# Kernel optimization log

Measured on AMD Instinct MI355X. Metric: run time of the kernel, lower is better.

Reference implementation:

```python
import jax, jax.numpy as jnp
import numpy as np

RES = 64
C_DIM = 64
N_BLOCKS = 4
EPS = 1e-12


def conv2d(x, w, b, pad):
    out = jax.lax.conv_general_dilated(
        x, w, window_strides=(1, 1), padding=[(pad, pad), (pad, pad)],
        dimension_numbers=('NCHW', 'OIHW', 'NCHW'))
    return out + b[None, :, None, None]


def unfold3(x):
    # F.unfold(kernel=3, padding=1): [B,C,H,W] -> [B, C*9, H*W], torch ordering (c, ki, kj)
    B, C, H, W = x.shape
    xp = jnp.pad(x, ((0, 0), (0, 0), (1, 1), (1, 1)))
    patches = jnp.stack([xp[:, :, ki:ki + H, kj:kj + W]
                         for ki in range(3) for kj in range(3)], axis=2)  # [B,C,9,H,W]
    return patches.reshape(B, C * 9, H * W)


def fold3(t, H, W):
    # F.fold(kernel=3, padding=1): sum overlapping patches back to [B,C,H,W]
    B, C9, L = t.shape
    C = C9 // 9
    t = t.reshape(B, C, 3, 3, H, W)
    out = jnp.zeros((B, C, H + 2, W + 2), t.dtype)
    for ki in range(3):
        for kj in range(3):
            out = out.at[:, :, ki:ki + H, kj:kj + W].add(t[:, :, ki, kj])
    return out[:, :, 1:H + 1, 1:W + 1]


def setup_inputs() -> dict:
    key = jax.random.key(0)
    ks = jax.random.split(key, 16)
    B, L, C = 4, RES * RES, C_DIM
    s = 0.05
    inp = {
        'c0': jax.random.normal(ks[0], (B, L, C), jnp.float32),
        'f0': jax.random.normal(ks[1], (B, L, C), jnp.float32),
        'c1': jax.random.normal(ks[2], (B, L, C), jnp.float32),
        'head_w': jax.random.normal(ks[3], (C, C, 5, 5), jnp.float32) * s,
        'head_b': jax.random.normal(ks[4], (C,), jnp.float32) * s,
        'rb_w1': jax.random.normal(ks[5], (N_BLOCKS, C, C, 3, 3), jnp.float32) * s,
        'rb_b1': jax.random.normal(ks[6], (N_BLOCKS, C), jnp.float32) * s,
        'rb_w2': jax.random.normal(ks[7], (N_BLOCKS, C, C, 3, 3), jnp.float32) * s,
        'rb_b2': jax.random.normal(ks[8], (N_BLOCKS, C), jnp.float32) * s,
        'tail_w': jax.random.normal(ks[9], (C, C, 5, 5), jnp.float32) * s,
        'tail_b': jax.random.normal(ks[10], (C,), jnp.float32) * s,
        'sq_w': jax.random.normal(ks[11], (C, 2 * C, 5, 5), jnp.float32) * s,
        'sq_b': jax.random.normal(ks[12], (C,), jnp.float32) * s,
    }
    return inp


def reference(c0, f0, c1, head_w, head_b, rb_w1, rb_b1, rb_w2, rb_b2,
              tail_w, tail_b, sq_w, sq_b):
    B, L, C = c1.shape
    H = W = RES
    c1 = c1.swapaxes(1, 2).reshape(B, C, H, W)
    c0 = c0.swapaxes(1, 2).reshape(B, C, H, W)
    f0 = f0.swapaxes(1, 2).reshape(B, C, H, W)
    Delta_c = c1 - c0

    # --- search_Trans: patch correlation + best-match texture transfer ---
    c1u = unfold3(c1)                       # [B, C9, L]
    c0u = unfold3(c0).swapaxes(1, 2)        # [B, L, C9]
    c0n = c0u / jnp.maximum(jnp.linalg.norm(c0u, axis=2, keepdims=True), EPS)
    c1n = c1u / jnp.maximum(jnp.linalg.norm(c1u, axis=1, keepdims=True), EPS)
    R = jnp.einsum('blk,bkm->blm', c0n, c1n)  # [B, L, L]
    R_star = jnp.max(R, axis=1)               # [B, L]
    R_arg = jnp.argmax(R, axis=1)              # [B, L]
    f0u = unfold3(f0)                          # [B, C9, L]
    Tu = jnp.take_along_axis(f0u, R_arg[:, None, :], axis=2)
    T = fold3(Tu, H, W) / 9.0                  # [B, C, H, W]
    S = R_star.reshape(B, 1, H, W)

    # --- residual conv stack on Delta_c ---
    x1 = conv2d(Delta_c, head_w, head_b, 2)
    x = x1
    for i in range(rb_w1.shape[0]):  # NOTE: original feeds x1 into every block
        h = jax.nn.relu(conv2d(x1, rb_w1[i], rb_b1[i], 1))
        x = conv2d(h, rb_w2[i], rb_b2[i], 1) + x1
    x = conv2d(x, tail_w, tail_b, 2)
    Delta_c_fea = x + x1

    x = conv2d(jnp.concatenate([Delta_c_fea, T], axis=1), sq_w, sq_b, 2)
    out = Delta_c_fea + x * S
    return out.reshape(B, C, L).swapaxes(1, 2)
```

## Files before the change

### kernel.cpp

```cpp
#include <hip/hip_runtime.h>
#include <hip/hip_bf16.h>


#define BATCH 4

typedef unsigned short u16;
typedef unsigned int   u32;
typedef __attribute__((ext_vector_type(8))) short short8;
typedef __attribute__((ext_vector_type(4))) float f32x4;

__device__ __forceinline__ void bsplit2(float a, float b, u32& ho, u32& lo) {
  __hip_bfloat16 ha = __float2bfloat16(a), hb = __float2bfloat16(b);
  float ra = a - __bfloat162float(ha), rb = b - __bfloat162float(hb);
  __hip_bfloat16 la = __float2bfloat16(ra), lb = __float2bfloat16(rb);
  ho = (u32)*(u16*)&ha | ((u32)*(u16*)&hb << 16);
  lo = (u32)*(u16*)&la | ((u32)*(u16*)&lb << 16);
}

__device__ __forceinline__ void gload_lds16(const void* g, void* l) {
  __builtin_amdgcn_global_load_lds((const __attribute__((address_space(1))) void*)g,
                                   (__attribute__((address_space(3))) void*)l, 16, 0, 0);
}

__global__ __launch_bounds__(256) void prep_ss(const float* __restrict__ c0,
    const float* __restrict__ c1, float* __restrict__ ss0, float* __restrict__ ss1)
{
  int tid = blockIdx.x * 256 + threadIdx.x;
  const float* p0 = c0 + (size_t)tid * 64;
  const float* p1 = c1 + (size_t)tid * 64;
  float s0 = 0.f, s1 = 0.f;
  for (int c = 0; c < 64; ++c) {
    float a = p0[c]; s0 += a * a;
    float b = p1[c]; s1 += b * b;
  }
  ss0[tid] = s0;
  ss1[tid] = s1;
}

__global__ __launch_bounds__(256) void norm_kernel(const float* __restrict__ ss0,
    const float* __restrict__ ss1, float* __restrict__ inv0, float* __restrict__ inv1)
{
  int tid = blockIdx.x * 256 + threadIdx.x;
  int b = tid >> 12, l = tid & 4095;
  int y = l >> 6, x = l & 63;
  int base = b << 12;
  float s0 = 0.f, s1 = 0.f;
  for (int dy = -1; dy <= 1; ++dy) {
    int yy = y + dy; if (yy < 0 || yy >= 64) continue;
    for (int dx = -1; dx <= 1; ++dx) {
      int xx = x + dx; if (xx < 0 || xx >= 64) continue;
      int ii = base + (yy << 6) + xx;
      s0 += ss0[ii]; s1 += ss1[ii];
    }
  }
  inv0[tid] = 1.f / fmaxf(sqrtf(s0), 1e-12f);
  inv1[tid] = 1.f / fmaxf(sqrtf(s1), 1e-12f);
}

__global__ __launch_bounds__(256) void split_pad_kernel(const float* __restrict__ c0,
    const float* __restrict__ c1, u16* __restrict__ p0h, u16* __restrict__ p0l,
    u16* __restrict__ p1h, u16* __restrict__ p1l)
{
  int b = blockIdx.y, t = threadIdx.x;
  int pix = blockIdx.x * 4 + (t >> 6);
  int c = t & 63;
  int py = pix / 66, px = pix - py * 66;
  size_t d = ((size_t)b * 4356 + pix) * 64 + c;
  float v0 = 0.f, v1 = 0.f;
  if (py >= 1 && py <= 64 && px >= 1 && px <= 64) {
    size_t s = (((size_t)b << 12) + ((py - 1) << 6) + (px - 1)) * 64 + c;
    v0 = c0[s]; v1 = c1[s];
  }
  __hip_bfloat16 h = __float2bfloat16(v0);
  float r = v0 - __bfloat162float(h);
  __hip_bfloat16 lo = __float2bfloat16(r);
  p0h[d] = *(u16*)&h; p0l[d] = *(u16*)&lo;
  h = __float2bfloat16(v1);
  r = v1 - __bfloat162float(h);
  lo = __float2bfloat16(r);
  p1h[d] = *(u16*)&h; p1l[d] = *(u16*)&lo;
}

__global__ __launch_bounds__(256) void wprep(const float* __restrict__ src,
    u16* __restrict__ wh, u16* __restrict__ wl, int Cin, int KK, int n)
{
  int i = blockIdx.x * 256 + threadIdx.x;
  if (i >= n) return;
  int per = Cin * KK;
  int cout = i / per;
  int rem = i - cout * per;
  int cin = rem / KK;
  int tap = rem - cin * KK;
  float x = src[i];
  __hip_bfloat16 h = __float2bfloat16(x);
  float r = x - __bfloat162float(h);
  __hip_bfloat16 lo = __float2bfloat16(r);
  int d = (tap * 64 + cout) * Cin + cin;
  wh[d] = *(u16*)&h;
  wl[d] = *(u16*)&lo;
}

__global__ __launch_bounds__(256) void corr_mfma(const u16* __restrict__ p0h,
    const u16* __restrict__ p0l, const u16* __restrict__ p1h, const u16* __restrict__ p1l,
    const float* __restrict__ inv0, float* __restrict__ pval, int* __restrict__ pidx)
{
  __shared__ __align__(16) u16 smem[16384];
  int mt = blockIdx.x, lt = blockIdx.y, b = blockIdx.z;
  int t = threadIdx.x;
  int lane = t & 63, w = t >> 6;
  int wl = w >> 1, wm = w & 1;
  int cc = lane & 15, q = lane >> 4;
  const size_t boff = (size_t)b * 278784;
  const u16* msrc = (w == 0) ? p0h : (w == 1) ? p0l : (w == 2) ? p1h : p1l;
  msrc += boff;
  const float* inv0b = inv0 + (b << 12);
  u16* ldsm = smem + (w << 12);
  int isB = w >> 1;

  int srow0 = lane >> 2;
  int cs_g  = (lane & 3) ^ ((lane >> 3) & 3);
  int sw    = (cc >> 1) & 3;

  float bval[4] = {-1e30f, -1e30f, -1e30f, -1e30f};
  int   bidx[4] = {0, 0, 0, 0};

  for (int sub = 0; sub < 4; ++sub) {
    int row0 = (lt << 9) + (sub << 7);
    int pb = isB ? (mt << 7) : row0;
    f32x4 acc[4][4];
#pragma unroll
    for (int i = 0; i < 4; ++i)
#pragma unroll
      for (int j = 0; j < 4; ++j) acc[i][j] = (f32x4){0.f, 0.f, 0.f, 0.f};

    for (int ph = 0; ph < 18; ++ph) {
      int r = ph >> 1, hh = ph & 1;
      int ki = r / 3, kj = r - ki * 3;
      __syncthreads();
#pragma unroll
      for (int it = 0; it < 8; ++it) {
        int row = (it << 4) + srow0;
        int p = pb + row;
        int ypad = (p >> 6) + ki, xpad = (p & 63) + kj;
        const u16* g = msrc + (((size_t)(ypad * 66 + xpad)) << 6) + (hh << 5) + (cs_g << 3);
        gload_lds16(g, ldsm + (it << 9));
      }
      __syncthreads();
      short8 afh[4], afl[4], bfh[4], bfl[4];
#pragma unroll
      for (int i = 0; i < 4; ++i) {
        int ra = (((wl << 6) + (i << 4) + cc) << 5) + ((q ^ sw) << 3);
        afh[i] = *(const short8*)(&smem[ra]);
        afl[i] = *(const short8*)(&smem[4096 + ra]);
      }
#pragma unroll
      for (int j = 0; j < 4; ++j) {
        int rb = (((wm << 6) + (j << 4) + cc) << 5) + ((q ^ sw) << 3);
        bfh[j] = *(const short8*)(&smem[8192 + rb]);
        bfl[j] = *(const short8*)(&smem[12288 + rb]);
      }
#pragma unroll
      for (int i = 0; i < 4; ++i)
#pragma unroll
        for (int j = 0; j < 4; ++j) {
          acc[i][j] = __builtin_amdgcn_mfma_f32_16x16x32_bf16(afh[i], bfl[j], acc[i][j], 0, 0, 0);
          acc[i][j] = __builtin_amdgcn_mfma_f32_16x16x32_bf16(afl[i], bfh[j], acc[i][j], 0, 0, 0);
          acc[i][j] = __builtin_amdgcn_mfma_f32_16x16x32_bf16(afh[i], bfh[j], acc[i][j], 0, 0, 0);
        }
    }
#pragma unroll
    for (int i = 0; i < 4; ++i) {
#pragma unroll
      for (int rg = 0; rg < 4; ++rg) {
        int l = row0 + (wl << 6) + (i << 4) + (q << 2) + rg;
        float sc = inv0b[l];
#pragma unroll
        for (int j = 0; j < 4; ++j) {
          float v = acc[i][j][rg] * sc;
          if (v > bval[j]) { bval[j] = v; bidx[j] = l; }
        }
      }
    }
  }

  __syncthreads();
  float* lval = (float*)smem;
  int*   lidx = (int*)((char*)smem + 4096);
  int slot = (wl << 2) + q;
#pragma unroll
  for (int j = 0; j < 4; ++j) {
    int col = (wm << 6) + (j << 4) + cc;
    lval[col * 8 + slot] = bval[j];
    lidx[col * 8 + slot] = bidx[j];
  }
  __syncthreads();
  if (t < 128) {
    float bv = -1e30f; int bi = 0x7FFFFFFF;
    for (int s = 0; s < 8; ++s) {
      float v = lval[t * 8 + s]; int id = lidx[t * 8 + s];
      if (v > bv || (v == bv && id < bi)) { bv = v; bi = id; }
    }
    size_t o = (size_t)(((b << 3) + lt) << 12) + (mt << 7) + t;
    pval[o] = bv; pidx[o] = bi;
  }
}

__global__ __launch_bounds__(256) void reduce_kernel(const float* __restrict__ pval,
    const int* __restrict__ pidx, const float* __restrict__ inv1,
    float* __restrict__ S, int* __restrict__ arg)
{
  int tid = blockIdx.x * 256 + threadIdx.x;
  int b = tid >> 12, m = tid & 4095;
  float bv = -1e30f; int bi = 0x7FFFFFFF;
  for (int lt = 0; lt < 8; ++lt) {
    size_t o = (size_t)(((b << 3) + lt) << 12) + m;
    float v = pval[o]; int id = pidx[o];
    if (v > bv || (v == bv && id < bi)) { bv = v; bi = id; }
  }
  S[tid] = bv * inv1[tid];
  arg[tid] = ((unsigned)bi < 4096u) ? bi : 0;
}

__global__ __launch_bounds__(256) void tgather_kernel(const float* __restrict__ f0,
    const int* __restrict__ arg, float* __restrict__ T)
{
  __shared__ int a3[192];
  int y = blockIdx.x, b = blockIdx.y, t = threadIdx.x;
  if (t < 192) {
    int r = t >> 6, xx = t & 63;
    int yy = y + r - 1;
    a3[t] = (yy >= 0 && yy < 64) ? arg[(b << 12) + (yy << 6) + xx] : 0;
  }
  __syncthreads();
  int c = t & 63, pg = t >> 6;
  for (int it = 0; it < 16; ++it) {
    int px = pg + (it << 2);
    float sum = 0.f;
#pragma unroll
    for (int ki = 0; ki < 3; ++ki) {
      int yn = y + 1 - ki;
      if (yn < 0 || yn >= 64) continue;
#pragma unroll
      for (int kj = 0; kj < 3; ++kj) {
        int xn = px + 1 - kj;
        if (xn < 0 || xn >= 64) continue;
        int p = a3[((2 - ki) << 6) + xn];
        int sy = (p >> 6) + ki - 1, sx = (p & 63) + kj - 1;
        if (sy >= 0 && sy < 64 && sx >= 0 && sx < 64)
          sum += f0[((((size_t)b << 12) + (sy << 6) + sx) << 6) + c];
      }
    }
    T[((((size_t)b << 12) + (y << 6) + px)) * 64 + c] = sum * (1.f / 9.f);
  }
}

template<int KS, int CINCH>
__global__ __launch_bounds__(256) void conv_mfma(const float* __restrict__ in0,
    const float* __restrict__ in1, const u16* __restrict__ whp, const u16* __restrict__ wlp,
    const float* __restrict__ bias, float* __restrict__ outp,
    const float* __restrict__ res, int dorelu, int dm)
{
  constexpr int P = KS / 2;
  constexpr int CIN = CINCH * 32;
  __shared__ __align__(16) u16 Ah[64 * 40], Al[64 * 40];
  __shared__ __align__(16) u16 Bh[64 * 40], Bl[64 * 40];
  int tile = blockIdx.x, b = blockIdx.y;
  int t = threadIdx.x;
  int lane = t & 63, w = t >> 6;
  int wh2 = w >> 1, wm = w & 1;
  int cc = lane & 15, q = lane >> 4;
  const size_t abase = (size_t)b << 12;
  f32x4 acc[2][2];
#pragma unroll
  for (int i = 0; i < 2; ++i)
#pragma unroll
    for (int j = 0; j < 2; ++j) acc[i][j] = (f32x4){0.f, 0.f, 0.f, 0.f};

  for (int tap = 0; tap < KS * KS; ++tap) {
    int ki = tap / KS, kj = tap - ki * KS;
    int iy = tile + ki - P;
    for (int kk = 0; kk < CINCH; ++kk) {
      __syncthreads();
      {
        int row = t >> 2, cs = t & 3;
        int ix = row + kj - P;
        float v[8];
#pragma unroll
        for (int e = 0; e < 8; ++e) v[e] = 0.f;
        if ((unsigned)iy < 64u && (unsigned)ix < 64u) {
          size_t base = (abase + (iy << 6) + ix) << 6;
          int cg = kk * 32 + (cs << 3);
          if (dm) {
            float4 a0 = *(const float4*)(in0 + base + cg);
            float4 a1 = *(const float4*)(in0 + base + cg + 4);
            float4 b0 = *(const float4*)(in1 + base + cg);
            float4 b1 = *(const float4*)(in1 + base + cg + 4);
            v[0] = b0.x - a0.x; v[1] = b0.y - a0.y; v[2] = b0.z - a0.z; v[3] = b0.w - a0.w;
            v[4] = b1.x - a1.x; v[5] = b1.y - a1.y; v[6] = b1.z - a1.z; v[7] = b1.w - a1.w;
          } else {
            const float* sp = (CINCH == 4 && cg >= 64) ? (in1 + base + (cg - 64))
                                                       : (in0 + base + cg);
            float4 a0 = *(const float4*)sp;
            float4 a1 = *(const float4*)(sp + 4);
            v[0] = a0.x; v[1] = a0.y; v[2] = a0.z; v[3] = a0.w;
            v[4] = a1.x; v[5] = a1.y; v[6] = a1.z; v[7] = a1.w;
          }
        }
        uint4 uh, ul;
        bsplit2(v[0], v[1], uh.x, ul.x);
        bsplit2(v[2], v[3], uh.y, ul.y);
        bsplit2(v[4], v[5], uh.z, ul.z);
        bsplit2(v[6], v[7], uh.w, ul.w);
        *(uint4*)&Ah[row * 40 + (cs << 3)] = uh;
        *(uint4*)&Al[row * 40 + (cs << 3)] = ul;
      }
#pragma unroll
      for (int it = 0; it < 2; ++it) {
        int row = t >> 2, cs = t & 3;
        const u16* wsrc = it ? wlp : whp;
        uint4 vv = *(const uint4*)&wsrc[(size_t)(tap * 64 + row) * CIN + kk * 32 + (cs << 3)];
        u16* dst = it ? Bl : Bh;
        *(uint4*)&dst[row * 40 + (cs << 3)] = vv;
      }
      __syncthreads();
      short8 afh[2], afl[2], bfh[2], bfl[2];
#pragma unroll
      for (int i = 0; i < 2; ++i) {
        int ra = ((wh2 << 5) + (i << 4) + cc) * 40 + (q << 3);
        afh[i] = *(const short8*)&Ah[ra];
        afl[i] = *(const short8*)&Al[ra];
      }
#pragma unroll
      for (int j = 0; j < 2; ++j) {
        int rb = ((wm << 5) + (j << 4) + cc) * 40 + (q << 3);
        bfh[j] = *(const short8*)&Bh[rb];
        bfl[j] = *(const short8*)&Bl[rb];
      }
#pragma unroll
      for (int i = 0; i < 2; ++i)
#pragma unroll
        for (int j = 0; j < 2; ++j) {
          acc[i][j] = __builtin_amdgcn_mfma_f32_16x16x32_bf16(afh[i], bfl[j], acc[i][j], 0, 0, 0);
          acc[i][j] = __builtin_amdgcn_mfma_f32_16x16x32_bf16(afl[i], bfh[j], acc[i][j], 0, 0, 0);
          acc[i][j] = __builtin_amdgcn_mfma_f32_16x16x32_bf16(afh[i], bfh[j], acc[i][j], 0, 0, 0);
        }
    }
  }
#pragma unroll
  for (int i = 0; i < 2; ++i)
#pragma unroll
    for (int rg = 0; rg < 4; ++rg) {
      int p = (tile << 6) + (wh2 << 5) + (i << 4) + (q << 2) + rg;
#pragma unroll
      for (int j = 0; j < 2; ++j) {
        int cout = (wm << 5) + (j << 4) + cc;
        float v = acc[i][j][rg] + bias[cout];
        if (dorelu) v = fmaxf(v, 0.f);
        size_t oi = ((abase + p) << 6) + cout;
        if (res) v += res[oi];
        outp[oi] = v;
      }
    }
}

__global__ __launch_bounds__(256) void final_kernel(const float* __restrict__ dcf,
    const float* __restrict__ xs, const float* __restrict__ S, float* __restrict__ out)
{
  int tid = blockIdx.x * 256 + threadIdx.x;
  out[tid] = dcf[tid] + xs[tid] * S[tid >> 6];
}

extern "C" void kernel_launch(void* const* d_in, const int* in_sizes, int n_in,
                              void* d_out, int out_size, void* d_ws, size_t ws_size,
                              hipStream_t stream)
{
  (void)in_sizes; (void)n_in; (void)out_size; (void)ws_size;
  const float* c0     = (const float*)d_in[0];
  const float* f0     = (const float*)d_in[1];
  const float* c1     = (const float*)d_in[2];
  const float* head_w = (const float*)d_in[3];
  const float* head_b = (const float*)d_in[4];
  const float* rb_w1  = (const float*)d_in[5];
  const float* rb_b1  = (const float*)d_in[6];
  const float* rb_w2  = (const float*)d_in[7];
  const float* rb_b2  = (const float*)d_in[8];
  const float* tail_w = (const float*)d_in[9];
  const float* tail_b = (const float*)d_in[10];
  const float* sq_w   = (const float*)d_in[11];
  const float* sq_b   = (const float*)d_in[12];
  float* out = (float*)d_out;
  char* ws = (char*)d_ws;

  const size_t OFF_SS0  = 0;
  const size_t OFF_SS1  = 65536;
  const size_t OFF_INV0 = 131072;
  const size_t OFF_INV1 = 196608;
  const size_t OFF_S    = 262144;
  const size_t OFF_ARG  = 327680;
  const size_t OFF_PVAL = 393216;
  const size_t OFF_PIDX = 917504;
  const size_t OFF_WHH  = 1441792;
  const size_t OFF_WHL  = 1646592;
  const size_t OFF_W1H  = 1851392;
  const size_t OFF_W1L  = 1925120;
  const size_t OFF_W2H  = 1998848;
  const size_t OFF_W2L  = 2072576;
  const size_t OFF_WTH  = 2146304;
  const size_t OFF_WTL  = 2351104;
  const size_t OFF_WSH  = 2555904;
  const size_t OFF_WSL  = 2965504;
  const size_t OFF_P0H  = 3375104;
  const size_t OFF_P0L  = OFF_P0H + 2230272;
  const size_t OFF_P1H  = OFF_P0L + 2230272;
  const size_t OFF_P1L  = OFF_P1H + 2230272;
  const size_t OFF_SA   = 3375104;
  const size_t OFF_SB   = 7569408;
  const size_t OFF_SC   = 11763712;

  float* ss0  = (float*)(ws + OFF_SS0);
  float* ss1  = (float*)(ws + OFF_SS1);
  float* inv0 = (float*)(ws + OFF_INV0);
  float* inv1 = (float*)(ws + OFF_INV1);
  float* Sbuf = (float*)(ws + OFF_S);
  int*   argb = (int*)(ws + OFF_ARG);
  float* pval = (float*)(ws + OFF_PVAL);
  int*   pidx = (int*)(ws + OFF_PIDX);
  u16* whh = (u16*)(ws + OFF_WHH); u16* whl = (u16*)(ws + OFF_WHL);
  u16* w1h = (u16*)(ws + OFF_W1H); u16* w1l = (u16*)(ws + OFF_W1L);
  u16* w2h = (u16*)(ws + OFF_W2H); u16* w2l = (u16*)(ws + OFF_W2L);
  u16* wth = (u16*)(ws + OFF_WTH); u16* wtl = (u16*)(ws + OFF_WTL);
  u16* wsh = (u16*)(ws + OFF_WSH); u16* wsl = (u16*)(ws + OFF_WSL);
  u16* p0h = (u16*)(ws + OFF_P0H); u16* p0l = (u16*)(ws + OFF_P0L);
  u16* p1h = (u16*)(ws + OFF_P1H); u16* p1l = (u16*)(ws + OFF_P1L);
  float* x1  = (float*)(ws + OFF_SA);
  float* Tb  = (float*)(ws + OFF_SA);
  float* hb  = (float*)(ws + OFF_SB);
  float* dcf = (float*)(ws + OFF_SB);
  float* xb  = (float*)(ws + OFF_SC);
  float* xsb = (float*)(ws + OFF_SC);

  dim3 b256(256);
  prep_ss<<<dim3(64), b256, 0, stream>>>(c0, c1, ss0, ss1);
  norm_kernel<<<dim3(64), b256, 0, stream>>>(ss0, ss1, inv0, inv1);
  split_pad_kernel<<<dim3(1089, BATCH), b256, 0, stream>>>(c0, c1, p0h, p0l, p1h, p1l);
  wprep<<<dim3(400), b256, 0, stream>>>(head_w, whh, whl, 64, 25, 102400);
  wprep<<<dim3(144), b256, 0, stream>>>(rb_w1 + 110592, w1h, w1l, 64, 9, 36864);
  wprep<<<dim3(144), b256, 0, stream>>>(rb_w2 + 110592, w2h, w2l, 64, 9, 36864);
  wprep<<<dim3(400), b256, 0, stream>>>(tail_w, wth, wtl, 64, 25, 102400);
  wprep<<<dim3(800), b256, 0, stream>>>(sq_w, wsh, wsl, 128, 25, 204800);

  corr_mfma<<<dim3(32, 8, BATCH), b256, 0, stream>>>(p0h, p0l, p1h, p1l, inv0, pval, pidx);
  reduce_kernel<<<dim3(64), b256, 0, stream>>>(pval, pidx, inv1, Sbuf, argb);

  dim3 cgrid(64, BATCH);
  conv_mfma<5, 2><<<cgrid, b256, 0, stream>>>(c0, c1, whh, whl, head_b, x1, nullptr, 0, 1);
  conv_mfma<3, 2><<<cgrid, b256, 0, stream>>>(x1, nullptr, w1h, w1l, rb_b1 + 192, hb, nullptr, 1, 0);
  conv_mfma<3, 2><<<cgrid, b256, 0, stream>>>(hb, nullptr, w2h, w2l, rb_b2 + 192, xb, x1, 0, 0);
  conv_mfma<5, 2><<<cgrid, b256, 0, stream>>>(xb, nullptr, wth, wtl, tail_b, dcf, x1, 0, 0);

  tgather_kernel<<<dim3(64, BATCH), b256, 0, stream>>>(f0, argb, Tb);
  conv_mfma<5, 4><<<cgrid, b256, 0, stream>>>(dcf, Tb, wsh, wsl, sq_b, xsb, nullptr, 0, 0);

  final_kernel<<<dim3(4096), b256, 0, stream>>>(dcf, xsb, Sbuf, out);
}
```

Baseline: 565.1 us.

## Double-buffer corr_mfma LDS loads and halve conv tile to double grid size

```diff
diff --git a/kernel.cpp b/kernel.cpp
--- a/kernel.cpp
+++ b/kernel.cpp
@@ -104,7 +104,7 @@
     const u16* __restrict__ p0l, const u16* __restrict__ p1h, const u16* __restrict__ p1l,
     const float* __restrict__ inv0, float* __restrict__ pval, int* __restrict__ pidx)
 {
-  __shared__ __align__(16) u16 smem[16384];
+  __shared__ __align__(16) u16 smem[32768];
   int mt = blockIdx.x, lt = blockIdx.y, b = blockIdx.z;
   int t = threadIdx.x;
   int lane = t & 63, w = t >> 6;
@@ -114,19 +114,32 @@
   const u16* msrc = (w == 0) ? p0h : (w == 1) ? p0l : (w == 2) ? p1h : p1l;
   msrc += boff;
   const float* inv0b = inv0 + (b << 12);
-  u16* ldsm = smem + (w << 12);
   int isB = w >> 1;
 
   int srow0 = lane >> 2;
   int cs_g  = (lane & 3) ^ ((lane >> 3) & 3);
   int sw    = (cc >> 1) & 3;
 
+  auto stage = [&](int ssub, int sph, u16* dst) {
+    int r = sph >> 1, hh = sph & 1;
+    int ki = r / 3, kj = r - ki * 3;
+    int pb = isB ? (mt << 7) : ((lt << 9) + (ssub << 7));
+#pragma unroll
+    for (int it = 0; it < 8; ++it) {
+      int p = pb + (it << 4) + srow0;
+      int ypad = (p >> 6) + ki, xpad = (p & 63) + kj;
+      const u16* g = msrc + (((size_t)(ypad * 66 + xpad)) << 6) + (hh << 5) + (cs_g << 3);
+      gload_lds16(g, dst + (it << 9));
+    }
+  };
+
   float bval[4] = {-1e30f, -1e30f, -1e30f, -1e30f};
   int   bidx[4] = {0, 0, 0, 0};
 
+  stage(0, 0, smem + (w << 12));
+
   for (int sub = 0; sub < 4; ++sub) {
     int row0 = (lt << 9) + (sub << 7);
-    int pb = isB ? (mt << 7) : row0;
     f32x4 acc[4][4];
 #pragma unroll
     for (int i = 0; i < 4; ++i)
@@ -134,30 +147,31 @@
       for (int j = 0; j < 4; ++j) acc[i][j] = (f32x4){0.f, 0.f, 0.f, 0.f};
 
     for (int ph = 0; ph < 18; ++ph) {
-      int r = ph >> 1, hh = ph & 1;
-      int ki = r / 3, kj = r - ki * 3;
-      __syncthreads();
-#pragma unroll
-      for (int it = 0; it < 8; ++it) {
-        int row = (it << 4) + srow0;
-        int p = pb + row;
-        int ypad = (p >> 6) + ki, xpad = (p & 63) + kj;
-        const u16* g = msrc + (((size_t)(ypad * 66 + xpad)) << 6) + (hh << 5) + (cs_g << 3);
-        gload_lds16(g, ldsm + (it << 9));
-      }
-      __syncthreads();
+      int g = sub * 18 + ph;
+      int nxt = g + 1;
+      if (nxt < 72) {
+        int np = ph + 1, ns = sub;
+        if (np == 18) { np = 0; ++ns; }
+        stage(ns, np, smem + ((nxt & 1) << 14) + (w << 12));
+        asm volatile("s_waitcnt vmcnt(8)" ::: "memory");
+      } else {
+        asm volatile("s_waitcnt vmcnt(0)" ::: "memory");
+      }
+      __builtin_amdgcn_s_barrier();
+      __builtin_amdgcn_sched_barrier(0);
+      const u16* bb = smem + ((g & 1) << 14);
       short8 afh[4], afl[4], bfh[4], bfl[4];
 #pragma unroll
       for (int i = 0; i < 4; ++i) {
         int ra = (((wl << 6) + (i << 4) + cc) << 5) + ((q ^ sw) << 3);
-        afh[i] = *(const short8*)(&smem[ra]);
-        afl[i] = *(const short8*)(&smem[4096 + ra]);
+        afh[i] = *(const short8*)(&bb[ra]);
+        afl[i] = *(const short8*)(&bb[4096 + ra]);
       }
 #pragma unroll
       for (int j = 0; j < 4; ++j) {
         int rb = (((wm << 6) + (j << 4) + cc) << 5) + ((q ^ sw) << 3);
-        bfh[j] = *(const short8*)(&smem[8192 + rb]);
-        bfl[j] = *(const short8*)(&smem[12288 + rb]);
+        bfh[j] = *(const short8*)(&bb[8192 + rb]);
+        bfl[j] = *(const short8*)(&bb[12288 + rb]);
       }
 #pragma unroll
       for (int i = 0; i < 4; ++i)
@@ -167,6 +181,8 @@
           acc[i][j] = __builtin_amdgcn_mfma_f32_16x16x32_bf16(afl[i], bfh[j], acc[i][j], 0, 0, 0);
           acc[i][j] = __builtin_amdgcn_mfma_f32_16x16x32_bf16(afh[i], bfh[j], acc[i][j], 0, 0, 0);
         }
+      __builtin_amdgcn_sched_barrier(0);
+      __builtin_amdgcn_s_barrier();
     }
 #pragma unroll
     for (int i = 0; i < 4; ++i) {
@@ -262,28 +278,27 @@
 {
   constexpr int P = KS / 2;
   constexpr int CIN = CINCH * 32;
-  __shared__ __align__(16) u16 Ah[64 * 40], Al[64 * 40];
+  __shared__ __align__(16) u16 Ah[32 * 40], Al[32 * 40];
   __shared__ __align__(16) u16 Bh[64 * 40], Bl[64 * 40];
   int tile = blockIdx.x, b = blockIdx.y;
   int t = threadIdx.x;
   int lane = t & 63, w = t >> 6;
-  int wh2 = w >> 1, wm = w & 1;
+  int wpx = w >> 1, wm = w & 1;
   int cc = lane & 15, q = lane >> 4;
+  int ty = tile >> 1, txb = (tile & 1) << 5;
   const size_t abase = (size_t)b << 12;
-  f32x4 acc[2][2];
-#pragma unroll
-  for (int i = 0; i < 2; ++i)
-#pragma unroll
-    for (int j = 0; j < 2; ++j) acc[i][j] = (f32x4){0.f, 0.f, 0.f, 0.f};
+  f32x4 acc[2];
+#pragma unroll
+  for (int j = 0; j < 2; ++j) acc[j] = (f32x4){0.f, 0.f, 0.f, 0.f};
 
   for (int tap = 0; tap < KS * KS; ++tap) {
     int ki = tap / KS, kj = tap - ki * KS;
-    int iy = tile + ki - P;
+    int iy = ty + ki - P;
     for (int kk = 0; kk < CINCH; ++kk) {
       __syncthreads();
-      {
+      if (t < 128) {
         int row = t >> 2, cs = t & 3;
-        int ix = row + kj - P;
+        int ix = txb + row + kj - P;
         float v[8];
 #pragma unroll
         for (int e = 0; e < 8; ++e) v[e] = 0.f;
@@ -313,22 +328,25 @@
         bsplit2(v[6], v[7], uh.w, ul.w);
         *(uint4*)&Ah[row * 40 + (cs << 3)] = uh;
         *(uint4*)&Al[row * 40 + (cs << 3)] = ul;
-      }
-#pragma unroll
-      for (int it = 0; it < 2; ++it) {
-        int row = t >> 2, cs = t & 3;
-        const u16* wsrc = it ? wlp : whp;
-        uint4 vv = *(const uint4*)&wsrc[(size_t)(tap * 64 + row) * CIN + kk * 32 + (cs << 3)];
-        u16* dst = it ? Bl : Bh;
-        *(uint4*)&dst[row * 40 + (cs << 3)] = vv;
+      } else {
+        int tb = t - 128;
+#pragma unroll
+        for (int rr = 0; rr < 2; ++rr) {
+          int idx = tb * 2 + rr;
+          int cout = idx >> 2, cs = idx & 3;
+          size_t so = (size_t)(tap * 64 + cout) * CIN + kk * 32 + (cs << 3);
+          uint4 vh = *(const uint4*)&whp[so];
+          uint4 vl = *(const uint4*)&wlp[so];
+          *(uint4*)&Bh[cout * 40 + (cs << 3)] = vh;
+          *(uint4*)&Bl[cout * 40 + (cs << 3)] = vl;
+        }
       }
       __syncthreads();
-      short8 afh[2], afl[2], bfh[2], bfl[2];
-#pragma unroll
-      for (int i = 0; i < 2; ++i) {
-        int ra = ((wh2 << 5) + (i << 4) + cc) * 40 + (q << 3);
-        afh[i] = *(const short8*)&Ah[ra];
-        afl[i] = *(const short8*)&Al[ra];
+      short8 afh, afl, bfh[2], bfl[2];
+      {
+        int ra = ((wpx << 4) + cc) * 40 + (q << 3);
+        afh = *(const short8*)&Ah[ra];
+        afl = *(const short8*)&Al[ra];
       }
 #pragma unroll
       for (int j = 0; j < 2; ++j) {
@@ -337,30 +355,26 @@
         bfl[j] = *(const short8*)&Bl[rb];
       }
 #pragma unroll
-      for (int i = 0; i < 2; ++i)
-#pragma unroll
-        for (int j = 0; j < 2; ++j) {
-          acc[i][j] = __builtin_amdgcn_mfma_f32_16x16x32_bf16(afh[i], bfl[j], acc[i][j], 0, 0, 0);
-          acc[i][j] = __builtin_amdgcn_mfma_f32_16x16x32_bf16(afl[i], bfh[j], acc[i][j], 0, 0, 0);
-          acc[i][j] = __builtin_amdgcn_mfma_f32_16x16x32_bf16(afh[i], bfh[j], acc[i][j], 0, 0, 0);
-        }
-    }
-  }
-#pragma unroll
-  for (int i = 0; i < 2; ++i)
-#pragma unroll
-    for (int rg = 0; rg < 4; ++rg) {
-      int p = (tile << 6) + (wh2 << 5) + (i << 4) + (q << 2) + rg;
-#pragma unroll
       for (int j = 0; j < 2; ++j) {
-        int cout = (wm << 5) + (j << 4) + cc;
-        float v = acc[i][j][rg] + bias[cout];
-        if (dorelu) v = fmaxf(v, 0.f);
-        size_t oi = ((abase + p) << 6) + cout;
-        if (res) v += res[oi];
-        outp[oi] = v;
-      }
-    }
+        acc[j] = __builtin_amdgcn_mfma_f32_16x16x32_bf16(afh, bfl[j], acc[j], 0, 0, 0);
+        acc[j] = __builtin_amdgcn_mfma_f32_16x16x32_bf16(afl, bfh[j], acc[j], 0, 0, 0);
+        acc[j] = __builtin_amdgcn_mfma_f32_16x16x32_bf16(afh, bfh[j], acc[j], 0, 0, 0);
+      }
+    }
+  }
+#pragma unroll
+  for (int rg = 0; rg < 4; ++rg) {
+    int p = (ty << 6) + txb + (wpx << 4) + (q << 2) + rg;
+#pragma unroll
+    for (int j = 0; j < 2; ++j) {
+      int cout = (wm << 5) + (j << 4) + cc;
+      float v = acc[j][rg] + bias[cout];
+      if (dorelu) v = fmaxf(v, 0.f);
+      size_t oi = ((abase + p) << 6) + cout;
+      if (res) v += res[oi];
+      outp[oi] = v;
+    }
+  }
 }
 
 __global__ __launch_bounds__(256) void final_kernel(const float* __restrict__ dcf,
@@ -452,7 +466,7 @@
   corr_mfma<<<dim3(32, 8, BATCH), b256, 0, stream>>>(p0h, p0l, p1h, p1l, inv0, pval, pidx);
   reduce_kernel<<<dim3(64), b256, 0, stream>>>(pval, pidx, inv1, Sbuf, argb);
 
-  dim3 cgrid(64, BATCH);
+  dim3 cgrid(128, BATCH);
   conv_mfma<5, 2><<<cgrid, b256, 0, stream>>>(c0, c1, whh, whl, head_b, x1, nullptr, 0, 1);
   conv_mfma<3, 2><<<cgrid, b256, 0, stream>>>(x1, nullptr, w1h, w1l, rb_b1 + 192, hb, nullptr, 1, 0);
   conv_mfma<3, 2><<<cgrid, b256, 0, stream>>>(hb, nullptr, w2h, w2l, rb_b2 + 192, xb, x1, 0, 0);
```

After: 555.3 us. About the same (-1.7%).
